# Optimization experiments

Hardware: AMD Instinct MI355X
Metric: run time of the kernel (lower is better)

The kernel has to match this reference:

```python
import jax, jax.numpy as jnp
import numpy as np
import math

EMSIZE = 256
NHEAD = 8
HEAD = EMSIZE // NHEAD
SEQ = 2048
BATCH = 2


def setup_inputs() -> dict:
    key = jax.random.key(0)
    ks = jax.random.split(key, 8)
    s = 1.0 / math.sqrt(EMSIZE)
    return {
        "em": jax.random.normal(ks[0], (SEQ, BATCH, EMSIZE), jnp.float32),
        "mask": jnp.zeros((BATCH, 1, SEQ, SEQ), jnp.float32),
        "Wq": jax.random.normal(ks[1], (EMSIZE, EMSIZE), jnp.float32) * s,
        "bq": jnp.zeros((EMSIZE,), jnp.float32),
        "Wk": jax.random.normal(ks[2], (EMSIZE, EMSIZE), jnp.float32) * s,
        "bk": jnp.zeros((EMSIZE,), jnp.float32),
        "Wv": jax.random.normal(ks[3], (EMSIZE, EMSIZE), jnp.float32) * s,
        "bv": jnp.zeros((EMSIZE,), jnp.float32),
    }


def reference(em, mask, Wq, bq, Wk, bk, Wv, bv):
    # em: [S, B, E] -> [B, S, E]
    x = jnp.swapaxes(em, 0, 1)
    B, S, E = x.shape
    H, D = NHEAD, HEAD
    # QKV projections (nn.Linear: x @ W.T + b), split heads -> [B, S, H, D]
    q = (x @ Wq.T + bq).reshape(B, S, H, D)
    k = (x @ Wk.T + bk).reshape(B, S, H, D)
    v = (x @ Wv.T + bv).reshape(B, S, H, D)
    # scores: [B, H, S, S]
    scores = jnp.einsum("bqhd,bkhd->bhqk", q, k) / math.sqrt(D) + mask
    attn = jax.nn.softmax(scores, axis=-1)  # dropout in eval mode = identity
    # context: [B, S, H, D] -> [B, S, E] -> [S, B, E]
    ctx = jnp.einsum("bhqk,bkhd->bqhd", attn, v).reshape(B, S, E)
    return jnp.swapaxes(ctx, 0, 1)
```

## Files before the change

### kernel.cpp

```cpp
#include <hip/hip_runtime.h>
#include <hip/hip_bf16.h>

typedef float f32x4 __attribute__((ext_vector_type(4)));
typedef float f32x16 __attribute__((ext_vector_type(16)));
typedef __bf16 bf16x8 __attribute__((ext_vector_type(8)));
typedef int v2i __attribute__((ext_vector_type(2)));
typedef unsigned short ushort_t;

#define SEQ 2048
#define BATCH 2
#define EMS 256
#define NHEAD 8
#define HEAD 32
#define BH (BATCH*NHEAD)
#define LOG2E 1.4426950408889634f
#define QSCALE 0.2550348211f
#define THRS 11.5415603f

static __device__ __forceinline__ ushort_t f2bfbits(float f) {
    unsigned int u = __float_as_uint(f);
    u += 0x7fffu + ((u >> 16) & 1u);
    return (ushort_t)(u >> 16);
}

static __device__ __forceinline__ unsigned cvtpk(float lo, float hi) {
    unsigned r;
    asm("v_cvt_pk_bf16_f32 %0, %1, %2" : "=v"(r) : "v"(lo), "v"(hi));
    return r;
}

static __device__ __forceinline__ float exp2a(float x) {
    float r;
    asm("v_exp_f32 %0, %1" : "=v"(r) : "v"(x));
    return r;
}

static __device__ __forceinline__ bf16x8 cvt8(const float* p) {
    float4 a = *reinterpret_cast<const float4*>(p);
    float4 b = *reinterpret_cast<const float4*>(p + 4);
    union { bf16x8 v; uint4 u; } x;
    x.u.x = cvtpk(a.x, a.y);
    x.u.y = cvtpk(a.z, a.w);
    x.u.z = cvtpk(b.x, b.y);
    x.u.w = cvtpk(b.z, b.w);
    return x.v;
}

__global__ __launch_bounds__(256) void fused_pre(
    const float* __restrict__ em, const float* __restrict__ mask,
    const float* __restrict__ Wq, const float* __restrict__ bq,
    const float* __restrict__ Wk, const float* __restrict__ bk,
    const float* __restrict__ Wv, const float* __restrict__ bv,
    ushort_t* __restrict__ Qb, ushort_t* __restrict__ Kb,
    ushort_t* __restrict__ Vb, unsigned* __restrict__ flagsG)
{
    if (blockIdx.x >= 384) {
        int sb = blockIdx.x - 384;
        int kh = sb & 1, qt = (sb >> 1) & 127, b = sb >> 8;
        int t = threadIdx.x;
        const float* base = mask + ((size_t)b * SEQ + qt * 16) * SEQ + kh * 1024 + t * 4;
        unsigned nz = 0;
        #pragma unroll 4
        for (int it = 0; it < 16; it++) {
            float4 v = *(const float4*)(base + (size_t)it * SEQ);
            unsigned u = (__float_as_uint(v.x) | __float_as_uint(v.y) |
                          __float_as_uint(v.z) | __float_as_uint(v.w)) << 1;
            if (u) nz = 1;
        }
        __shared__ unsigned fl;
        if (t == 0) fl = 0;
        __syncthreads();
        if (nz) atomicOr(&fl, 1u << (t >> 3));
        __syncthreads();
        if (t == 0) flagsG[(b * 128 + qt) * 2 + kh] = fl;
        return;
    }

    int wid = blockIdx.x * 4 + (threadIdx.x >> 6);
    int l   = threadIdx.x & 63;
    int l15 = l & 15, lq = l >> 4;
    int rb = wid / 12, cg = wid % 12;
    int r0 = rb * 32, c0 = cg * 64;
    int sel = c0 >> 8;
    const float* W    = sel == 0 ? Wq : (sel == 1 ? Wk : Wv);
    const float* bias = sel == 0 ? bq : (sel == 1 ? bk : bv);
    ushort_t*    dst  = sel == 0 ? Qb : (sel == 1 ? Kb : Vb);
    int cb = c0 & 255;

    f32x4 acc[2][4];
    #pragma unroll
    for (int m = 0; m < 2; m++)
        #pragma unroll
        for (int n = 0; n < 4; n++) acc[m][n] = (f32x4){0.f, 0.f, 0.f, 0.f};

    #pragma unroll
    for (int kk = 0; kk < 8; kk++) {
        int k0 = kk * 32;
        bf16x8 af[2], bfm[4];
        #pragma unroll
        for (int m = 0; m < 2; m++)
            af[m] = cvt8(em + (size_t)(r0 + m * 16 + l15) * EMS + k0 + lq * 8);
        #pragma unroll
        for (int n = 0; n < 4; n++)
            bfm[n] = cvt8(W + (size_t)(cb + n * 16 + l15) * EMS + k0 + lq * 8);
        #pragma unroll
        for (int m = 0; m < 2; m++)
            #pragma unroll
            for (int n = 0; n < 4; n++)
                acc[m][n] = __builtin_amdgcn_mfma_f32_16x16x32_bf16(af[m], bfm[n], acc[m][n], 0, 0, 0);
    }

    float scale = (sel == 0) ? QSCALE : 1.0f;
    #pragma unroll
    for (int m = 0; m < 2; m++) {
        #pragma unroll
        for (int n = 0; n < 4; n++) {
            int c = cb + n * 16 + l15;
            float bv_ = bias[c];
            int h = c >> 5, d = c & 31;
            #pragma unroll
            for (int r = 0; r < 4; r++) {
                int row = r0 + m * 16 + lq * 4 + r;
                int s = row >> 1, b = row & 1;
                ushort_t v = f2bfbits((acc[m][n][r] + bv_) * scale);
                dst[((size_t)(b * NHEAD + h) * SEQ + s) * HEAD + d] = v;
            }
        }
    }
}

__global__ __launch_bounds__(256) void vtrans(const ushort_t* __restrict__ Vb,
                                              ushort_t* __restrict__ Vt2)
{
    __shared__ ushort_t t[HEAD][65];
    int g = blockIdx.x;
    int bh = g & 15, st = g >> 4;
    int s0 = st * 64;
    int tid = threadIdx.x;
    #pragma unroll
    for (int i = 0; i < 8; i++) {
        int idx = i * 256 + tid;
        int sl = idx >> 5, d = idx & 31;
        t[d][sl] = Vb[((size_t)bh * SEQ + s0 + sl) * HEAD + d];
    }
    __syncthreads();
    #pragma unroll
    for (int i = 0; i < 8; i++) {
        int idx = i * 256 + tid;
        int kb_l = idx >> 10, rem = idx & 1023;
        int d = rem >> 5, si = rem & 31;
        Vt2[(((size_t)bh * 64 + (s0 >> 5) + kb_l) * 32 + d) * 32 + si] = t[d][kb_l * 32 + si];
    }
}

__global__ __launch_bounds__(256, 4) void attn(
    const ushort_t* __restrict__ Qb, const ushort_t* __restrict__ Kb,
    const ushort_t* __restrict__ Vt2, const float* __restrict__ mask,
    const unsigned long long* __restrict__ flagsG, float* __restrict__ out)
{
    int g  = blockIdx.x;
    int qt = g >> 4;
    int b  = (g >> 3) & 1;
    int h  = g & 7;
    int bh = b * NHEAD + h;
    int w  = threadIdx.x >> 6;
    int l  = threadIdx.x & 63;
    int l31 = l & 31, hi = l >> 5;
    int qs0 = qt * 32;

    __shared__ float oacc[4][32][36];
    __shared__ float om[4][32], ol[4][32];

    const ushort_t* qrow = Qb + ((size_t)bh * SEQ + qs0 + l31) * HEAD + hi * 8;
    bf16x8 qf0 = *(const bf16x8*)(qrow);
    bf16x8 qf1 = *(const bf16x8*)(qrow + 16);

    unsigned long long fbits = flagsG[b * 128 + qt * 2] | flagsG[b * 128 + qt * 2 + 1];

    f32x16 acc = {};
    float mrun = -1e30f, lsum = 0.f;

    int k0 = w * (SEQ / 4);
    const ushort_t* kbase = Kb  + ((size_t)bh * SEQ + k0 + l31) * HEAD + hi * 8;
    const ushort_t* vbase = Vt2 + ((size_t)bh * 64 + (k0 >> 5)) * 1024 + l31 * 32 + hi * 8;

    bf16x8 kc0 = *(const bf16x8*)(kbase);
    bf16x8 kc1 = *(const bf16x8*)(kbase + 16);
    bf16x8 vc0 = *(const bf16x8*)(vbase);
    bf16x8 vc1 = *(const bf16x8*)(vbase + 16);

    const int NT = (SEQ / 4) / 32;
    for (int kt = 0; kt < NT; kt++) {
        int ktn = (kt + 1 < NT) ? kt + 1 : 0;
        f32x16 st = {};
        st = __builtin_amdgcn_mfma_f32_32x32x16_bf16(kc0, qf0, st, 0, 0, 0);
        st = __builtin_amdgcn_mfma_f32_32x32x16_bf16(kc1, qf1, st, 0, 0, 0);

        bf16x8 kn0 = *(const bf16x8*)(kbase + ktn * 1024);
        bf16x8 kn1 = *(const bf16x8*)(kbase + ktn * 1024 + 16);
        bf16x8 vn0 = *(const bf16x8*)(vbase + ktn * 1024);
        bf16x8 vn1 = *(const bf16x8*)(vbase + ktn * 1024 + 16);

        if ((fbits >> (w * 16 + kt)) & 1ull) {
            const float* mr = mask + (size_t)b * SEQ * SEQ
                            + (size_t)(qs0 + l31) * SEQ + k0 + kt * 32 + hi * 4;
            union { float4 f4[4]; float f[16]; } mu;
            mu.f4[0] = *(const float4*)(mr);
            mu.f4[1] = *(const float4*)(mr + 8);
            mu.f4[2] = *(const float4*)(mr + 16);
            mu.f4[3] = *(const float4*)(mr + 24);
            #pragma unroll
            for (int j = 0; j < 16; j++) st[j] += mu.f[j] * LOG2E;
        }

        float x0 = fmaxf(st[0], st[1]),  x1 = fmaxf(st[2], st[3]);
        float x2 = fmaxf(st[4], st[5]),  x3 = fmaxf(st[6], st[7]);
        float x4 = fmaxf(st[8], st[9]),  x5 = fmaxf(st[10], st[11]);
        float x6 = fmaxf(st[12], st[13]), x7 = fmaxf(st[14], st[15]);
        float lmax = fmaxf(fmaxf(fmaxf(x0, x1), fmaxf(x2, x3)),
                           fmaxf(fmaxf(x4, x5), fmaxf(x6, x7)));

        if (__any(lmax > mrun + THRS)) {
            v2i sw = __builtin_amdgcn_permlane32_swap(
                __float_as_int(lmax), __float_as_int(lmax), false, false);
            float pm = fmaxf(fmaxf(lmax, __int_as_float(sw.x)), __int_as_float(sw.y));
            float nm = fmaxf(mrun, pm);
            float sc = exp2a(mrun - nm);
            lsum *= sc;
            #pragma unroll
            for (int j = 0; j < 16; j++) acc[j] *= sc;
            mrun = nm;
        }

        float ev[16];
        #pragma unroll
        for (int j = 0; j < 16; j++) ev[j] = exp2a(st[j] - mrun);
        lsum += (((ev[0]+ev[1])+(ev[2]+ev[3])) + ((ev[4]+ev[5])+(ev[6]+ev[7])))
              + (((ev[8]+ev[9])+(ev[10]+ev[11])) + ((ev[12]+ev[13])+(ev[14]+ev[15])));

        unsigned pk[8];
        #pragma unroll
        for (int j = 0; j < 8; j++) pk[j] = cvtpk(ev[2 * j], ev[2 * j + 1]);
        v2i p0 = __builtin_amdgcn_permlane32_swap((int)pk[0], (int)pk[2], false, false);
        v2i p1 = __builtin_amdgcn_permlane32_swap((int)pk[1], (int)pk[3], false, false);
        v2i p2 = __builtin_amdgcn_permlane32_swap((int)pk[4], (int)pk[6], false, false);
        v2i p3 = __builtin_amdgcn_permlane32_swap((int)pk[5], (int)pk[7], false, false);
        union { int i[4]; bf16x8 v; } pf0, pf1;
        pf0.i[0] = p0.x; pf0.i[1] = p1.x; pf0.i[2] = p0.y; pf0.i[3] = p1.y;
        pf1.i[0] = p2.x; pf1.i[1] = p3.x; pf1.i[2] = p2.y; pf1.i[3] = p3.y;

        acc = __builtin_amdgcn_mfma_f32_32x32x16_bf16(vc0, pf0.v, acc, 0, 0, 0);
        acc = __builtin_amdgcn_mfma_f32_32x32x16_bf16(vc1, pf1.v, acc, 0, 0, 0);

        kc0 = kn0; kc1 = kn1; vc0 = vn0; vc1 = vn1;
    }

    v2i sl = __builtin_amdgcn_permlane32_swap(
        __float_as_int(lsum), __float_as_int(lsum), false, false);
    float lt = __int_as_float(sl.x) + __int_as_float(sl.y);
    if (hi == 0) { om[w][l31] = mrun; ol[w][l31] = lt; }

    #pragma unroll
    for (int gg = 0; gg < 4; gg++) {
        f32x4 vv = { acc[4*gg], acc[4*gg+1], acc[4*gg+2], acc[4*gg+3] };
        *(f32x4*)&oacc[w][l31][8 * gg + 4 * hi] = vv;
    }
    __syncthreads();

    int t = threadIdx.x;
    int q = t >> 3, d4 = (t & 7) * 4;
    float m0 = om[0][q], m1 = om[1][q], m2 = om[2][q], m3 = om[3][q];
    float mg = fmaxf(fmaxf(m0, m1), fmaxf(m2, m3));
    float w0_ = exp2a(m0 - mg), w1_ = exp2a(m1 - mg);
    float w2_ = exp2a(m2 - mg), w3_ = exp2a(m3 - mg);
    float lg = w0_ * ol[0][q] + w1_ * ol[1][q] + w2_ * ol[2][q] + w3_ * ol[3][q];
    float inv = 1.0f / lg;
    float4 o;
    o.x = (w0_*oacc[0][q][d4]   + w1_*oacc[1][q][d4]   + w2_*oacc[2][q][d4]   + w3_*oacc[3][q][d4])   * inv;
    o.y = (w0_*oacc[0][q][d4+1] + w1_*oacc[1][q][d4+1] + w2_*oacc[2][q][d4+1] + w3_*oacc[3][q][d4+1]) * inv;
    o.z = (w0_*oacc[0][q][d4+2] + w1_*oacc[1][q][d4+2] + w2_*oacc[2][q][d4+2] + w3_*oacc[3][q][d4+2]) * inv;
    o.w = (w0_*oacc[0][q][d4+3] + w1_*oacc[1][q][d4+3] + w2_*oacc[2][q][d4+3] + w3_*oacc[3][q][d4+3]) * inv;
    *(float4*)(out + ((size_t)(qs0 + q) * BATCH + b) * EMS + h * HEAD + d4) = o;
}

extern "C" void kernel_launch(void* const* d_in, const int* in_sizes, int n_in,
                              void* d_out, int out_size, void* d_ws, size_t ws_size,
                              hipStream_t stream) {
    const float* em  = (const float*)d_in[0];
    const float* mask = (const float*)d_in[1];
    const float* Wq  = (const float*)d_in[2];
    const float* bq  = (const float*)d_in[3];
    const float* Wk  = (const float*)d_in[4];
    const float* bk  = (const float*)d_in[5];
    const float* Wv  = (const float*)d_in[6];
    const float* bv  = (const float*)d_in[7];
    float* out = (float*)d_out;

    ushort_t* Qb  = (ushort_t*)d_ws;
    ushort_t* Kb  = Qb + (size_t)BH * SEQ * HEAD;
    ushort_t* Vb  = Kb + (size_t)BH * SEQ * HEAD;
    ushort_t* Vt2 = Vb + (size_t)BH * SEQ * HEAD;
    unsigned* flagsG = (unsigned*)(Vt2 + (size_t)BH * SEQ * HEAD);

    fused_pre<<<dim3(896), dim3(256), 0, stream>>>(em, mask, Wq, bq, Wk, bk, Wv, bv,
                                                   Qb, Kb, Vb, flagsG);
    vtrans<<<dim3(512), dim3(256), 0, stream>>>(Vb, Vt2);
    attn<<<dim3(1024), dim3(256), 0, stream>>>(Qb, Kb, Vt2, mask,
                                               (const unsigned long long*)flagsG, out);
}
```

Baseline: 51.71 us.

## Split mask scan into own kernel, vectorize V transpose, batch mask loads

Moves the mask-nonzero scan out of the fused projection kernel into a separate mask_scan kernel that issues all 16 float4 loads up front before reducing. The V transpose now uses 16-byte vector loads and stores through a padded shared tile instead of scalar 2-byte accesses. The intent is to raise memory-level parallelism on the 32MB mask read and cut transpose instruction count. The cost is one extra kernel launch and the loss of overlap between the mask scan and the projection blocks.

```diff
diff --git a/kernel.cpp b/kernel.cpp
--- a/kernel.cpp
+++ b/kernel.cpp
@@ -46,36 +46,14 @@
     return x.v;
 }
 
-__global__ __launch_bounds__(256) void fused_pre(
-    const float* __restrict__ em, const float* __restrict__ mask,
+__global__ __launch_bounds__(256) void qkv_proj(
+    const float* __restrict__ em,
     const float* __restrict__ Wq, const float* __restrict__ bq,
     const float* __restrict__ Wk, const float* __restrict__ bk,
     const float* __restrict__ Wv, const float* __restrict__ bv,
     ushort_t* __restrict__ Qb, ushort_t* __restrict__ Kb,
-    ushort_t* __restrict__ Vb, unsigned* __restrict__ flagsG)
+    ushort_t* __restrict__ Vb)
 {
-    if (blockIdx.x >= 384) {
-        int sb = blockIdx.x - 384;
-        int kh = sb & 1, qt = (sb >> 1) & 127, b = sb >> 8;
-        int t = threadIdx.x;
-        const float* base = mask + ((size_t)b * SEQ + qt * 16) * SEQ + kh * 1024 + t * 4;
-        unsigned nz = 0;
-        #pragma unroll 4
-        for (int it = 0; it < 16; it++) {
-            float4 v = *(const float4*)(base + (size_t)it * SEQ);
-            unsigned u = (__float_as_uint(v.x) | __float_as_uint(v.y) |
-                          __float_as_uint(v.z) | __float_as_uint(v.w)) << 1;
-            if (u) nz = 1;
-        }
-        __shared__ unsigned fl;
-        if (t == 0) fl = 0;
-        __syncthreads();
-        if (nz) atomicOr(&fl, 1u << (t >> 3));
-        __syncthreads();
-        if (t == 0) flagsG[(b * 128 + qt) * 2 + kh] = fl;
-        return;
-    }
-
     int wid = blockIdx.x * 4 + (threadIdx.x >> 6);
     int l   = threadIdx.x & 63;
     int l15 = l & 15, lq = l >> 4;
@@ -132,25 +110,52 @@
 __global__ __launch_bounds__(256) void vtrans(const ushort_t* __restrict__ Vb,
                                               ushort_t* __restrict__ Vt2)
 {
-    __shared__ ushort_t t[HEAD][65];
+    __shared__ ushort_t t[64][40];
     int g = blockIdx.x;
     int bh = g & 15, st = g >> 4;
     int s0 = st * 64;
     int tid = threadIdx.x;
-    #pragma unroll
-    for (int i = 0; i < 8; i++) {
-        int idx = i * 256 + tid;
-        int sl = idx >> 5, d = idx & 31;
-        t[d][sl] = Vb[((size_t)bh * SEQ + s0 + sl) * HEAD + d];
+
+    {
+        int sl = tid >> 2, d0 = (tid & 3) * 8;
+        uint4 v = *(const uint4*)(Vb + ((size_t)bh * SEQ + s0 + sl) * HEAD + d0);
+        *(uint4*)&t[sl][d0] = v;
     }
     __syncthreads();
-    #pragma unroll
-    for (int i = 0; i < 8; i++) {
-        int idx = i * 256 + tid;
-        int kb_l = idx >> 10, rem = idx & 1023;
-        int d = rem >> 5, si = rem & 31;
-        Vt2[(((size_t)bh * 64 + (s0 >> 5) + kb_l) * 32 + d) * 32 + si] = t[d][kb_l * 32 + si];
-    }
+    {
+        int kb_l = tid >> 7, rem = tid & 127;
+        int d = rem >> 2, si0 = (rem & 3) * 8;
+        union { ushort_t u[8]; uint4 q; } o;
+        #pragma unroll
+        for (int j = 0; j < 8; j++) o.u[j] = t[kb_l * 32 + si0 + j][d];
+        *(uint4*)(Vt2 + (((size_t)bh * 64 + (s0 >> 5) + kb_l) * 32 + d) * 32 + si0) = o.q;
+    }
+}
+
+__global__ __launch_bounds__(256, 2) void mask_scan(
+    const float* __restrict__ mask, unsigned* __restrict__ flagsG)
+{
+    int sb = blockIdx.x;
+    int kh = sb & 1, qt = (sb >> 1) & 127, b = sb >> 8;
+    int t = threadIdx.x;
+    const float* base = mask + ((size_t)b * SEQ + qt * 16) * SEQ + kh * 1024 + t * 4;
+    float4 v[16];
+    #pragma unroll
+    for (int it = 0; it < 16; it++)
+        v[it] = *(const float4*)(base + (size_t)it * SEQ);
+    unsigned acc = 0;
+    #pragma unroll
+    for (int it = 0; it < 16; it++)
+        acc |= __float_as_uint(v[it].x) | __float_as_uint(v[it].y)
+             | __float_as_uint(v[it].z) | __float_as_uint(v[it].w);
+    unsigned nz = (acc & 0x7fffffffu) != 0u;
+
+    __shared__ unsigned fl;
+    if (t == 0) fl = 0;
+    __syncthreads();
+    if (nz) atomicOr(&fl, 1u << (t >> 3));
+    __syncthreads();
+    if (t == 0) flagsG[(b * 128 + qt) * 2 + kh] = fl;
 }
 
 __global__ __launch_bounds__(256, 4) void attn(
@@ -302,9 +307,9 @@
     ushort_t* Vt2 = Vb + (size_t)BH * SEQ * HEAD;
     unsigned* flagsG = (unsigned*)(Vt2 + (size_t)BH * SEQ * HEAD);
 
-    fused_pre<<<dim3(896), dim3(256), 0, stream>>>(em, mask, Wq, bq, Wk, bk, Wv, bv,
-                                                   Qb, Kb, Vb, flagsG);
+    qkv_proj<<<dim3(384), dim3(256), 0, stream>>>(em, Wq, bq, Wk, bk, Wv, bv, Qb, Kb, Vb);
     vtrans<<<dim3(512), dim3(256), 0, stream>>>(Vb, Vt2);
+    mask_scan<<<dim3(512), dim3(256), 0, stream>>>(mask, flagsG);
     attn<<<dim3(1024), dim3(256), 0, stream>>>(Qb, Kb, Vt2, mask,
                                                (const unsigned long long*)flagsG, out);
 }
```

Result: slower. 57.18 us (+10.6%).
